# Performance work log

Hardware: AMD Instinct MI355X
Metric: run time of the kernel (lower is better)

Reference implementation:

```python
import jax, jax.numpy as jnp
import numpy as np

B, N, C_IN, HID, K, DEG = 8192, 64, 128, 128, 5, 8


def setup_inputs() -> dict:
    key = jax.random.key(0)
    ks = jax.random.split(key, 8)
    total = B * N
    E = B * N * DEG
    x = jax.random.normal(ks[0], (total, C_IN), dtype=jnp.float32)
    batch = jnp.repeat(jnp.arange(B, dtype=jnp.int64), N)
    g = jnp.repeat(jnp.arange(B, dtype=jnp.int64), N * DEG)
    src = g * N + jax.random.randint(ks[1], (E,), 0, N).astype(jnp.int64)
    dst = g * N + jax.random.randint(ks[2], (E,), 0, N).astype(jnp.int64)
    edge_index = jnp.stack([src, dst])  # [2, E]
    s = 0.05
    return {
        "x": x,
        "edge_index": edge_index,
        "batch": batch,
        "W_pool": jax.random.normal(ks[3], (C_IN, K), dtype=jnp.float32) * s,
        "b_pool": jnp.zeros((K,), jnp.float32),
        "W1": jax.random.normal(ks[4], (C_IN, HID), dtype=jnp.float32) * s,
        "b1": jnp.zeros((HID,), jnp.float32),
        "W2": jax.random.normal(ks[5], (HID, HID), dtype=jnp.float32) * s,
        "b2": jnp.zeros((HID,), jnp.float32),
        "W_lin": jax.random.normal(ks[6], (HID, 1), dtype=jnp.float32) * s,
        "b_lin": jnp.zeros((1,), jnp.float32),
        "num_graphs": B,
        "max_nodes": N,
    }


def dense_gcn(x, adj, W, b, mask=None):
    # PyG DenseGCNConv with add_loop=True: diagonal set to 1 on a copy
    n = adj.shape[1]
    idx = jnp.arange(n)
    adj_l = adj.at[:, idx, idx].set(1.0)
    out = x @ W  # [B, n, out]
    d = jnp.clip(adj_l.sum(-1), 1.0) ** -0.5  # [B, n]
    adj_n = d[:, :, None] * adj_l * d[:, None, :]
    out = jnp.einsum('bnm,bmc->bnc', adj_n, out) + b
    if mask is not None:
        out = out * mask[..., None]
    return out


def reference(x, edge_index, batch, W_pool, b_pool, W1, b1, W2, b2, W_lin, b_lin,
              num_graphs, max_nodes):
    total = x.shape[0]
    # to_dense_batch: position of each node within its graph (batch is sorted)
    first_idx = jax.ops.segment_min(jnp.arange(total), batch, num_segments=num_graphs)
    pos = jnp.arange(total) - first_idx[batch]
    x_dense = jnp.zeros((num_graphs, max_nodes, x.shape[1]), x.dtype).at[batch, pos].set(x)
    mask = jnp.zeros((num_graphs, max_nodes), x.dtype).at[batch, pos].set(1.0)
    # to_dense_adj
    src, dst = edge_index[0], edge_index[1]
    adj = jnp.zeros((num_graphs, max_nodes, max_nodes), x.dtype)
    adj = adj.at[batch[src], pos[src], pos[dst]].add(1.0)

    s = dense_gcn(x_dense, adj, W_pool, b_pool, mask)       # [B, N, K]
    x_l1 = dense_gcn(x_dense, adj, W1, b1, mask)            # [B, N, H]

    # dense_diff_pool (losses are discarded by the original forward)
    s = jax.nn.softmax(s, axis=-1) * mask[..., None]
    xm = x_l1 * mask[..., None]
    x_p1 = jnp.einsum('bnk,bnc->bkc', s, xm)                # [B, K, H]
    adj_p1 = jnp.einsum('bnk,bnm,bml->bkl', s, adj, s)      # [B, K, K]

    x_l2 = dense_gcn(x_p1, adj_p1, W2, b2)                  # [B, K, H]
    pooled = x_l2.sum(axis=1)                               # global_add_pool -> [B, H]
    return pooled @ W_lin + b_lin                           # [B, 1]
```

## Files before the change

### kernel.cpp

```cpp
#include <hip/hip_runtime.h>
#include <hip/hip_bf16.h>

#define NN 64
#define CI 128
#define HD 128
#define KC 5
#define SXS 136

#define WS_Z   9216
#define WS_B1Z 9344
#define WS_B2W 9345

typedef float v4f __attribute__((ext_vector_type(4)));
typedef __bf16 v8bf __attribute__((ext_vector_type(8)));
typedef unsigned short us8 __attribute__((ext_vector_type(8)));

__device__ __forceinline__ float us2f(unsigned short u) {
    union { unsigned i; float f; } v; v.i = ((unsigned)u) << 16; return v.f;
}
__device__ __forceinline__ unsigned short f2us(float f) {
    __hip_bfloat16 h = __float2bfloat16(f);
    return *reinterpret_cast<unsigned short*>(&h);
}

extern "C" __global__ void zprep(const float* __restrict__ W1,
                                 const float* __restrict__ Wp,
                                 const float* __restrict__ W2,
                                 const float* __restrict__ Wl,
                                 const float* __restrict__ b1,
                                 const float* __restrict__ b2,
                                 float* __restrict__ ws)
{
    const int b = blockIdx.x, t = threadIdx.x;
    if (b < 36) {
        const int ct = b >> 2, ks = b & 3;
        const int q = t >> 4, m16 = t & 15;
        const int k0 = ks * 32 + q * 8;
        us8 pk;
        #pragma unroll
        for (int j = 0; j < 8; ++j) {
            const int k = k0 + j;
            float v;
            if (ct < 8)      v = W1[k * HD + ct * 16 + m16];
            else             v = (m16 < KC) ? Wp[k * KC + m16] : 0.f;
            pk[j] = f2us(v);
        }
        reinterpret_cast<us8*>(ws)[b * 64 + t] = pk;
    } else if (b == 36) {
        float a0 = 0.f, a1 = 0.f;
        for (int c = 0; c < HD; ++c) {
            const float wl = Wl[c];
            a0 += W2[t * HD + c] * wl;
            a1 += W2[(t + 64) * HD + c] * wl;
        }
        ws[WS_Z + t] = a0;
        ws[WS_Z + 64 + t] = a1;
        float p1 = b1[t] * a0 + b1[t + 64] * a1;
        float p2 = b2[t] * Wl[t] + b2[t + 64] * Wl[t + 64];
        #pragma unroll
        for (int off = 32; off; off >>= 1) {
            p1 += __shfl_down(p1, off, 64);
            p2 += __shfl_down(p2, off, 64);
        }
        if (t == 0) { ws[WS_B1Z] = p1; ws[WS_B2W] = p2; }
    }
}

extern "C" __global__ __launch_bounds__(256, 4)
void diffpool_main(const float* __restrict__ x,
                   const int* __restrict__ ei,
                   const float* __restrict__ bp,
                   const float* __restrict__ bl,
                   const float* __restrict__ ws,
                   float* __restrict__ out,
                   int E, int epg)
{
    __shared__ __attribute__((aligned(16))) unsigned short sx[NN][SXS];
    __shared__ int   sadj[NN][NN + 1];
    __shared__ float sS0[NN][KC];
    __shared__ float sS [NN][KC];
    __shared__ float sU [NN][KC];
    __shared__ float sd [NN];
    __shared__ float sz [HD];
    __shared__ float sqp[2][NN];
    __shared__ float sw_[NN];
    __shared__ float sadjp[25];
    __shared__ float sd2[KC];
    __shared__ float scoef[KC];

    const int t = threadIdx.x;
    const int g = blockIdx.x;
    const int lane = t & 63;
    const int wv = t >> 6;

    {
        int* ap = &sadj[0][0];
        for (int i = t; i < NN * (NN + 1); i += 256) ap[i] = 0;
        const float* xg = x + (size_t)g * (NN * CI);
        #pragma unroll
        for (int i = 0; i < 4; ++i) {
            const int idx = t + 256 * i;
            const int row = idx >> 4, ch = idx & 15;
            const float4 v0 = *reinterpret_cast<const float4*>(xg + row * CI + ch * 8);
            const float4 v1 = *reinterpret_cast<const float4*>(xg + row * CI + ch * 8 + 4);
            us8 pk;
            pk[0] = f2us(v0.x); pk[1] = f2us(v0.y); pk[2] = f2us(v0.z); pk[3] = f2us(v0.w);
            pk[4] = f2us(v1.x); pk[5] = f2us(v1.y); pk[6] = f2us(v1.z); pk[7] = f2us(v1.w);
            *reinterpret_cast<us8*>(&sx[row][ch * 8]) = pk;
        }
        if (t < 32)
            reinterpret_cast<float4*>(sz)[t] = reinterpret_cast<const float4*>(ws + WS_Z)[t];
    }
    __syncthreads();

    {
        const int base = g * epg;
        for (int j = t; j < epg; j += 256) {
            const int sn = ei[base + j] & 63;
            const int dn = ei[E + base + j] & 63;
            atomicAdd(&sadj[sn][dn], 1);
        }
    }
    __syncthreads();

    {
        const int m16 = lane & 15;
        const int q = lane >> 4;
        const int arow = wv * 16 + m16;
        v8bf afrag[4];
        #pragma unroll
        for (int ks = 0; ks < 4; ++ks)
            afrag[ks] = *reinterpret_cast<const v8bf*>(&sx[arow][ks * 32 + q * 8]);
        const v8bf* wpk = reinterpret_cast<const v8bf*>(ws);
        #pragma unroll
        for (int ct = 0; ct < 9; ++ct) {
            v4f acc = {0.f, 0.f, 0.f, 0.f};
            #pragma unroll
            for (int ks = 0; ks < 4; ++ks) {
                const v8bf bfrag = wpk[(ct * 4 + ks) * 64 + lane];
                acc = __builtin_amdgcn_mfma_f32_16x16x32_bf16(afrag[ks], bfrag, acc, 0, 0, 0);
            }
            if (ct < 8) {
                #pragma unroll
                for (int r = 0; r < 4; ++r)
                    sx[wv * 16 + q * 4 + r][ct * 16 + m16] = f2us(acc[r]);
            } else if (m16 < KC) {
                #pragma unroll
                for (int r = 0; r < 4; ++r)
                    sS0[wv * 16 + q * 4 + r][m16] = acc[r];
            }
        }
    }
    if (t < NN) {
        int si = 0;
        for (int m = 0; m < NN; ++m) si += sadj[t][m];
        const int deg = si + 1 - sadj[t][t];
        sd[t] = rsqrtf((float)deg);
    }
    __syncthreads();

    float sv0 = 0.f, sv1 = 0.f, sv2 = 0.f, sv3 = 0.f, sv4 = 0.f;

    if (wv == 0) {
        const int n = lane;
        const float dn = sd[n];
        float a0 = 0.f, a1 = 0.f, a2 = 0.f, a3 = 0.f, a4 = 0.f;
        for (int m = 0; m < NN; ++m) {
            const float al = (m == n) ? 1.f : (float)sadj[n][m];
            const float f = al * sd[m];
            a0 += f * sS0[m][0]; a1 += f * sS0[m][1]; a2 += f * sS0[m][2];
            a3 += f * sS0[m][3]; a4 += f * sS0[m][4];
        }
        a0 = a0 * dn + bp[0]; a1 = a1 * dn + bp[1]; a2 = a2 * dn + bp[2];
        a3 = a3 * dn + bp[3]; a4 = a4 * dn + bp[4];
        const float mx = fmaxf(fmaxf(fmaxf(a0, a1), fmaxf(a2, a3)), a4);
        a0 = expf(a0 - mx); a1 = expf(a1 - mx); a2 = expf(a2 - mx);
        a3 = expf(a3 - mx); a4 = expf(a4 - mx);
        const float inv = 1.f / (a0 + a1 + a2 + a3 + a4);
        sv0 = a0 * inv; sv1 = a1 * inv; sv2 = a2 * inv; sv3 = a3 * inv; sv4 = a4 * inv;
        sS[n][0] = sv0; sS[n][1] = sv1; sS[n][2] = sv2; sS[n][3] = sv3; sS[n][4] = sv4;
        float u0 = 0.f, u1 = 0.f, u2 = 0.f, u3 = 0.f, u4 = 0.f;
        for (int m = 0; m < NN; ++m) {
            const float a = (float)sadj[n][m];
            u0 += a * sS[m][0]; u1 += a * sS[m][1]; u2 += a * sS[m][2];
            u3 += a * sS[m][3]; u4 += a * sS[m][4];
        }
        sU[n][0] = u0; sU[n][1] = u1; sU[n][2] = u2; sU[n][3] = u3; sU[n][4] = u4;
        if (n < 25) {
            const int k = n / 5, l = n % 5;
            float a = 0.f;
            for (int mm = 0; mm < NN; ++mm) a += sS[mm][k] * sU[mm][l];
            sadjp[n] = a;
        }
        if (n < KC) {
            float s_ = 0.f;
            #pragma unroll
            for (int l = 0; l < KC; ++l) s_ += sadjp[n * 5 + l];
            s_ += 1.f - sadjp[n * 6];
            sd2[n] = rsqrtf(fmaxf(s_, 1.f));
        }
        if (n < KC) {
            float a = 0.f;
            #pragma unroll
            for (int k = 0; k < KC; ++k) a += sd2[k] * sadjp[k * 5 + n];
            a += sd2[n] * (1.f - sadjp[n * 6]);
            scoef[n] = sd2[n] * a;
        }
        const float wn = dn * (scoef[0] * sv0 + scoef[1] * sv1 + scoef[2] * sv2 +
                               scoef[3] * sv3 + scoef[4] * sv4);
        sw_[n] = wn;
    } else if (wv <= 2) {
        const int p = wv - 1, m = lane;
        float a = 0.f;
        #pragma unroll
        for (int c = 0; c < 8; ++c) {
            const us8 h = *reinterpret_cast<const us8*>(&sx[m][p * 64 + c * 8]);
            #pragma unroll
            for (int j = 0; j < 8; ++j) a += us2f(h[j]) * sz[p * 64 + c * 8 + j];
        }
        sqp[p][m] = a;
    }
    __syncthreads();

    if (wv == 0) {
        const int m = lane;
        float a = 0.f;
        for (int n = 0; n < NN; ++n) {
            const float al = (n == m) ? 1.f : (float)sadj[n][m];
            a += sw_[n] * al;
        }
        const float qm = sqp[0][m] + sqp[1][m];
        float v = sd[m] * a * qm;
        v += (scoef[0] * sv0 + scoef[1] * sv1 + scoef[2] * sv2 +
              scoef[3] * sv3 + scoef[4] * sv4) * ws[WS_B1Z];
        #pragma unroll
        for (int off = 32; off; off >>= 1) v += __shfl_down(v, off, 64);
        if (lane == 0)
            out[g] = v + 5.f * ws[WS_B2W] + bl[0];
    }
}

extern "C" void kernel_launch(void* const* d_in, const int* in_sizes, int n_in,
                              void* d_out, int out_size, void* d_ws, size_t ws_size,
                              hipStream_t stream) {
    const float* x  = (const float*)d_in[0];
    const int*   ei = (const int*)d_in[1];
    const float* Wp = (const float*)d_in[3];
    const float* bp = (const float*)d_in[4];
    const float* W1 = (const float*)d_in[5];
    const float* b1 = (const float*)d_in[6];
    const float* W2 = (const float*)d_in[7];
    const float* b2 = (const float*)d_in[8];
    const float* Wl = (const float*)d_in[9];
    const float* bl = (const float*)d_in[10];
    float* out = (float*)d_out;
    float* ws  = (float*)d_ws;

    const int B = out_size;
    const int E = in_sizes[1] / 2;
    const int epg = E / B;

    zprep<<<37, 64, 0, stream>>>(W1, Wp, W2, Wl, b1, b2, ws);
    diffpool_main<<<B, 256, 0, stream>>>(x, ei, bp, bl, ws, out, E, epg);
}
```

Baseline: 492.7 us.

## Pack adjacency into bytes and split graph reductions across all four waves

Stores the per-graph adjacency as packed 8-bit counts, which shrinks the LDS footprint, and keeps a separate atomic row-degree counter so the degree no longer needs a row sum. The serial single-wave loops over 64 neighbours (S propagation, adj*S, the pooled adjacency and the final column sum) are split so each of the four waves handles 16 columns, with partial sums reduced through shared memory. Edge indices are prefetched before the LDS clear, and launch bounds are raised to 5 blocks per CU. This adds extra barriers and assumes edge multiplicity per pair stays below 256.

Measured after the change: 474.1 us. 1.04x faster.

```diff
diff --git a/kernel.cpp b/kernel.cpp
--- a/kernel.cpp
+++ b/kernel.cpp
@@ -6,6 +6,7 @@
 #define HD 128
 #define KC 5
 #define SXS 136
+#define AJW 17
 
 #define WS_Z   9216
 #define WS_B1Z 9344
@@ -66,7 +67,7 @@
     }
 }
 
-extern "C" __global__ __launch_bounds__(256, 4)
+extern "C" __global__ __launch_bounds__(256, 5)
 void diffpool_main(const float* __restrict__ x,
                    const int* __restrict__ ei,
                    const float* __restrict__ bp,
@@ -76,26 +77,35 @@
                    int E, int epg)
 {
     __shared__ __attribute__((aligned(16))) unsigned short sx[NN][SXS];
-    __shared__ int   sadj[NN][NN + 1];
-    __shared__ float sS0[NN][KC];
-    __shared__ float sS [NN][KC];
-    __shared__ float sU [NN][KC];
-    __shared__ float sd [NN];
+    __shared__ unsigned int sadjb[NN][AJW];
+    __shared__ float sSm[NN][KC];
+    __shared__ float spart[4][NN * KC];
     __shared__ float sz [HD];
     __shared__ float sqp[2][NN];
+    __shared__ float sd [NN];
     __shared__ float sw_[NN];
+    __shared__ unsigned int srdeg[NN];
+    __shared__ float spp[4][25];
     __shared__ float sadjp[25];
     __shared__ float sd2[KC];
-    __shared__ float scoef[KC];
+    __shared__ float scoef[KC + 1];
 
     const int t = threadIdx.x;
     const int g = blockIdx.x;
     const int lane = t & 63;
     const int wv = t >> 6;
-
-    {
-        int* ap = &sadj[0][0];
-        for (int i = t; i < NN * (NN + 1); i += 256) ap[i] = 0;
+    const int n = lane;
+    const int h = wv;
+
+    int e0s = -1, e0d = 0, e1s = -1, e1d = 0;
+    const int base = g * epg;
+    if (t < epg)       { e0s = ei[base + t] & 63;        e0d = ei[E + base + t] & 63; }
+    if (t + 256 < epg) { e1s = ei[base + t + 256] & 63;  e1d = ei[E + base + t + 256] & 63; }
+
+    {
+        unsigned int* ap = &sadjb[0][0];
+        for (int i = t; i < NN * AJW; i += 256) ap[i] = 0u;
+        if (t < NN) srdeg[t] = 0u;
         const float* xg = x + (size_t)g * (NN * CI);
         #pragma unroll
         for (int i = 0; i < 4; ++i) {
@@ -114,11 +124,19 @@
     __syncthreads();
 
     {
-        const int base = g * epg;
-        for (int j = t; j < epg; j += 256) {
+        if (e0s >= 0) {
+            atomicAdd(&sadjb[e0s][e0d >> 2], 1u << ((e0d & 3) * 8));
+            atomicAdd(&srdeg[e0s], 1u);
+        }
+        if (e1s >= 0) {
+            atomicAdd(&sadjb[e1s][e1d >> 2], 1u << ((e1d & 3) * 8));
+            atomicAdd(&srdeg[e1s], 1u);
+        }
+        for (int j = t + 512; j < epg; j += 256) {
             const int sn = ei[base + j] & 63;
             const int dn = ei[E + base + j] & 63;
-            atomicAdd(&sadj[sn][dn], 1);
+            atomicAdd(&sadjb[sn][dn >> 2], 1u << ((dn & 3) * 8));
+            atomicAdd(&srdeg[sn], 1u);
         }
     }
     __syncthreads();
@@ -147,96 +165,143 @@
             } else if (m16 < KC) {
                 #pragma unroll
                 for (int r = 0; r < 4; ++r)
-                    sS0[wv * 16 + q * 4 + r][m16] = acc[r];
+                    sSm[wv * 16 + q * 4 + r][m16] = acc[r];
             }
         }
     }
     if (t < NN) {
-        int si = 0;
-        for (int m = 0; m < NN; ++m) si += sadj[t][m];
-        const int deg = si + 1 - sadj[t][t];
-        sd[t] = rsqrtf((float)deg);
-    }
-    __syncthreads();
-
-    float sv0 = 0.f, sv1 = 0.f, sv2 = 0.f, sv3 = 0.f, sv4 = 0.f;
+        const unsigned self = (sadjb[t][t >> 2] >> ((t & 3) * 8)) & 255u;
+        sd[t] = rsqrtf((float)(srdeg[t] + 1u - self));
+    }
+    __syncthreads();
+
+    {
+        float a0 = 0.f, a1 = 0.f, a2 = 0.f, a3 = 0.f, a4 = 0.f;
+        #pragma unroll
+        for (int i = 0; i < 4; ++i) {
+            const unsigned w = sadjb[n][h * 4 + i];
+            #pragma unroll
+            for (int b = 0; b < 4; ++b) {
+                const int m = h * 16 + i * 4 + b;
+                const float al = (m == n) ? 1.f : (float)((w >> (b * 8)) & 255u);
+                const float f = al * sd[m];
+                a0 += f * sSm[m][0]; a1 += f * sSm[m][1]; a2 += f * sSm[m][2];
+                a3 += f * sSm[m][3]; a4 += f * sSm[m][4];
+            }
+        }
+        float* pp = &spart[h][n * KC];
+        pp[0] = a0; pp[1] = a1; pp[2] = a2; pp[3] = a3; pp[4] = a4;
+    }
+    __syncthreads();
 
     if (wv == 0) {
-        const int n = lane;
+        float a0 = spart[0][n*KC+0] + spart[1][n*KC+0] + spart[2][n*KC+0] + spart[3][n*KC+0];
+        float a1 = spart[0][n*KC+1] + spart[1][n*KC+1] + spart[2][n*KC+1] + spart[3][n*KC+1];
+        float a2 = spart[0][n*KC+2] + spart[1][n*KC+2] + spart[2][n*KC+2] + spart[3][n*KC+2];
+        float a3 = spart[0][n*KC+3] + spart[1][n*KC+3] + spart[2][n*KC+3] + spart[3][n*KC+3];
+        float a4 = spart[0][n*KC+4] + spart[1][n*KC+4] + spart[2][n*KC+4] + spart[3][n*KC+4];
         const float dn = sd[n];
-        float a0 = 0.f, a1 = 0.f, a2 = 0.f, a3 = 0.f, a4 = 0.f;
-        for (int m = 0; m < NN; ++m) {
-            const float al = (m == n) ? 1.f : (float)sadj[n][m];
-            const float f = al * sd[m];
-            a0 += f * sS0[m][0]; a1 += f * sS0[m][1]; a2 += f * sS0[m][2];
-            a3 += f * sS0[m][3]; a4 += f * sS0[m][4];
-        }
         a0 = a0 * dn + bp[0]; a1 = a1 * dn + bp[1]; a2 = a2 * dn + bp[2];
         a3 = a3 * dn + bp[3]; a4 = a4 * dn + bp[4];
         const float mx = fmaxf(fmaxf(fmaxf(a0, a1), fmaxf(a2, a3)), a4);
         a0 = expf(a0 - mx); a1 = expf(a1 - mx); a2 = expf(a2 - mx);
         a3 = expf(a3 - mx); a4 = expf(a4 - mx);
         const float inv = 1.f / (a0 + a1 + a2 + a3 + a4);
-        sv0 = a0 * inv; sv1 = a1 * inv; sv2 = a2 * inv; sv3 = a3 * inv; sv4 = a4 * inv;
-        sS[n][0] = sv0; sS[n][1] = sv1; sS[n][2] = sv2; sS[n][3] = sv3; sS[n][4] = sv4;
-        float u0 = 0.f, u1 = 0.f, u2 = 0.f, u3 = 0.f, u4 = 0.f;
-        for (int m = 0; m < NN; ++m) {
-            const float a = (float)sadj[n][m];
-            u0 += a * sS[m][0]; u1 += a * sS[m][1]; u2 += a * sS[m][2];
-            u3 += a * sS[m][3]; u4 += a * sS[m][4];
-        }
-        sU[n][0] = u0; sU[n][1] = u1; sU[n][2] = u2; sU[n][3] = u3; sU[n][4] = u4;
-        if (n < 25) {
-            const int k = n / 5, l = n % 5;
-            float a = 0.f;
-            for (int mm = 0; mm < NN; ++mm) a += sS[mm][k] * sU[mm][l];
-            sadjp[n] = a;
-        }
-        if (n < KC) {
-            float s_ = 0.f;
-            #pragma unroll
-            for (int l = 0; l < KC; ++l) s_ += sadjp[n * 5 + l];
-            s_ += 1.f - sadjp[n * 6];
-            sd2[n] = rsqrtf(fmaxf(s_, 1.f));
-        }
-        if (n < KC) {
-            float a = 0.f;
-            #pragma unroll
-            for (int k = 0; k < KC; ++k) a += sd2[k] * sadjp[k * 5 + n];
-            a += sd2[n] * (1.f - sadjp[n * 6]);
-            scoef[n] = sd2[n] * a;
-        }
-        const float wn = dn * (scoef[0] * sv0 + scoef[1] * sv1 + scoef[2] * sv2 +
-                               scoef[3] * sv3 + scoef[4] * sv4);
-        sw_[n] = wn;
+        sSm[n][0] = a0 * inv; sSm[n][1] = a1 * inv; sSm[n][2] = a2 * inv;
+        sSm[n][3] = a3 * inv; sSm[n][4] = a4 * inv;
     } else if (wv <= 2) {
         const int p = wv - 1, m = lane;
         float a = 0.f;
         #pragma unroll
-        for (int c = 0; c < 8; ++c) {
-            const us8 h = *reinterpret_cast<const us8*>(&sx[m][p * 64 + c * 8]);
-            #pragma unroll
-            for (int j = 0; j < 8; ++j) a += us2f(h[j]) * sz[p * 64 + c * 8 + j];
+        for (int cc = 0; cc < 8; ++cc) {
+            const int c = (cc + (m >> 3)) & 7;
+            const us8 hh = *reinterpret_cast<const us8*>(&sx[m][p * 64 + c * 8]);
+            #pragma unroll
+            for (int j = 0; j < 8; ++j) a += us2f(hh[j]) * sz[p * 64 + c * 8 + j];
         }
         sqp[p][m] = a;
     }
     __syncthreads();
 
+    {
+        float u0 = 0.f, u1 = 0.f, u2 = 0.f, u3 = 0.f, u4 = 0.f;
+        #pragma unroll
+        for (int i = 0; i < 4; ++i) {
+            const unsigned w = sadjb[n][h * 4 + i];
+            #pragma unroll
+            for (int b = 0; b < 4; ++b) {
+                const int m = h * 16 + i * 4 + b;
+                const float c = (float)((w >> (b * 8)) & 255u);
+                u0 += c * sSm[m][0]; u1 += c * sSm[m][1]; u2 += c * sSm[m][2];
+                u3 += c * sSm[m][3]; u4 += c * sSm[m][4];
+            }
+        }
+        float* pp = &spart[h][n * KC];
+        pp[0] = u0; pp[1] = u1; pp[2] = u2; pp[3] = u3; pp[4] = u4;
+    }
+    __syncthreads();
+
+    if (lane < 25) {
+        const int k = lane / 5, l = lane - k * 5;
+        float a = 0.f;
+        #pragma unroll
+        for (int i = 0; i < 16; ++i) {
+            const int m = h * 16 + i;
+            const float u = spart[0][m*KC+l] + spart[1][m*KC+l] +
+                            spart[2][m*KC+l] + spart[3][m*KC+l];
+            a += sSm[m][k] * u;
+        }
+        spp[h][lane] = a;
+    }
+    __syncthreads();
+
     if (wv == 0) {
-        const int m = lane;
-        float a = 0.f;
-        for (int n = 0; n < NN; ++n) {
-            const float al = (n == m) ? 1.f : (float)sadj[n][m];
-            a += sw_[n] * al;
-        }
-        const float qm = sqp[0][m] + sqp[1][m];
-        float v = sd[m] * a * qm;
-        v += (scoef[0] * sv0 + scoef[1] * sv1 + scoef[2] * sv2 +
-              scoef[3] * sv3 + scoef[4] * sv4) * ws[WS_B1Z];
+        if (lane < 25)
+            sadjp[lane] = spp[0][lane] + spp[1][lane] + spp[2][lane] + spp[3][lane];
+        if (lane < KC) {
+            float s_ = 0.f;
+            #pragma unroll
+            for (int l = 0; l < KC; ++l) s_ += sadjp[lane * KC + l];
+            s_ += 1.f - sadjp[lane * 6];
+            sd2[lane] = rsqrtf(fmaxf(s_, 1.f));
+        }
+        if (lane < KC) {
+            float a = 0.f;
+            #pragma unroll
+            for (int k = 0; k < KC; ++k) a += sd2[k] * sadjp[k * KC + lane];
+            a += sd2[lane] * (1.f - sadjp[lane * 6]);
+            scoef[lane] = sd2[lane] * a;
+        }
+        float t5 = scoef[0] * sSm[n][0] + scoef[1] * sSm[n][1] + scoef[2] * sSm[n][2] +
+                   scoef[3] * sSm[n][3] + scoef[4] * sSm[n][4];
+        sw_[n] = sd[n] * t5;
+        #pragma unroll
+        for (int off = 32; off; off >>= 1) t5 += __shfl_down(t5, off, 64);
+        if (lane == 0) scoef[KC] = t5;
+    }
+    __syncthreads();
+
+    {
+        float pa = 0.f;
+        #pragma unroll
+        for (int i = 0; i < 16; ++i) {
+            const int nn2 = h * 16 + i;
+            const float al = (nn2 == n) ? 1.f
+                           : (float)((sadjb[nn2][n >> 2] >> ((n & 3) * 8)) & 255u);
+            pa += sw_[nn2] * al;
+        }
+        spart[h][n] = pa;
+    }
+    __syncthreads();
+
+    if (wv == 0) {
+        const float a = spart[0][n] + spart[1][n] + spart[2][n] + spart[3][n];
+        const float qm = sqp[0][n] + sqp[1][n];
+        float v = sd[n] * a * qm;
         #pragma unroll
         for (int off = 32; off; off >>= 1) v += __shfl_down(v, off, 64);
         if (lane == 0)
-            out[g] = v + 5.f * ws[WS_B2W] + bl[0];
+            out[g] = v + scoef[KC] * ws[WS_B1Z] + 5.f * ws[WS_B2W] + bl[0];
     }
 }
 
```
